# Kernel optimization log

Hardware: AMD Instinct MI355X
Metric: run time of the kernel (lower is better)

## Reference

```python
import jax, jax.numpy as jnp
import numpy as np

B, T = 16384, 512          # batch, seq_len
DSTATE, DINPUT = 4, 4       # quaternion state / quaternion input
DMLP1, DMLP2 = 128, 128     # ODEFunc MLP hidden widths


def _linear_params(key, fan_in, fan_out):
    # torch nn.Linear default init: U(-1/sqrt(fan_in), 1/sqrt(fan_in))
    lim = 1.0 / np.sqrt(fan_in)
    kw, kb = jax.random.split(key)
    W = jax.random.uniform(kw, (fan_in, fan_out), jnp.float32, -lim, lim)
    b = jax.random.uniform(kb, (fan_out,), jnp.float32, -lim, lim)
    return W, b


def setup_inputs() -> dict:
    key = jax.random.key(0)
    k1, k2, k3, kx = jax.random.split(key, 4)
    W1, b1 = _linear_params(k1, DSTATE + DINPUT, DMLP1)
    W2, b2 = _linear_params(k2, DMLP1, DMLP2)
    W3, b3 = _linear_params(k3, DMLP2, DSTATE)
    quat_seq = jax.random.normal(kx, (B, T, DINPUT), jnp.float32)
    return {"quat_seq": quat_seq, "W1": W1, "b1": b1, "W2": W2, "b2": b2,
            "W3": W3, "b3": b3}


def reference(quat_seq, W1, b1, W2, b2, W3, b3):
    batch = quat_seq.shape[0]
    dstate = W3.shape[1]

    def odefunc(h, q):
        # f(t, [h, q]) -> dh/dt ; time is unused by the net
        x = jnp.concatenate([h, q], axis=-1)            # [B, DSTATE+DINPUT]
        x = jax.nn.silu(x @ W1 + b1)                    # [B, DMLP1]
        x = jax.nn.silu(x @ W2 + b2)                    # [B, DMLP2]
        return x @ W3 + b3                              # [B, DSTATE]

    dt = 1.0  # t_span = [0, 1] on a fixed grid -> single RK4 step of size 1

    def step(h, q_t):
        # torchdiffeq fixed-grid 'rk4' uses the 3/8-rule (rk4_alt_step_func)
        k1 = odefunc(h, q_t)
        k2 = odefunc(h + dt * k1 / 3.0, q_t)
        k3 = odefunc(h + dt * (k2 - k1 / 3.0), q_t)
        k4 = odefunc(h + dt * (k1 - k2 + k3), q_t)
        h_new = h + dt * (k1 + 3.0 * (k2 + k3) + k4) / 8.0
        return h_new, None

    h0 = jnp.zeros((batch, dstate), quat_seq.dtype).at[:, 0].set(1.0)
    # scan over time: [T, B, DINPUT]
    h_final, _ = jax.lax.scan(step, h0, jnp.swapaxes(quat_seq, 0, 1))
    return h_final
```

## Files before the change

### kernel.cpp

```cpp
#include <hip/hip_runtime.h>
#include <hip/hip_bf16.h>

typedef float f32x4  __attribute__((ext_vector_type(4)));
typedef float f32x16 __attribute__((ext_vector_type(16)));
typedef short short8v __attribute__((ext_vector_type(8)));
typedef unsigned int uint;

constexpr int TSTEPS = 512;

union FragU { uint u[4]; short8v v; };

__device__ __forceinline__ float silu_f(float x) {
    return __fdividef(x, 1.0f + __expf(-x));
}

__device__ __forceinline__ uint bf16_rne(float x) {
    uint ux = __float_as_uint(x);
    return (ux + 0x7FFFu + ((ux >> 16) & 1u)) & 0xFFFF0000u;
}
__device__ __forceinline__ void split2u(float x, uint &h, uint &l) {
    h = bf16_rne(x);
    float rem = x - __uint_as_float(h);
    l = bf16_rne(rem);
}

__device__ __forceinline__ uint cvtpk(float a, float b) {
    union { __hip_bfloat162 h; uint u; } cv;
    cv.h = __float22bfloat162_rn(make_float2(a, b));
    return cv.u;
}
__device__ __forceinline__ void split4_pk(const f32x4 v, uint2 &hi, uint2 &lo) {
    hi.x = cvtpk(v.x, v.y);
    hi.y = cvtpk(v.z, v.w);
    float h0 = __uint_as_float(hi.x << 16);
    float h1 = __uint_as_float(hi.x & 0xFFFF0000u);
    float h2 = __uint_as_float(hi.y << 16);
    float h3 = __uint_as_float(hi.y & 0xFFFF0000u);
    lo.x = cvtpk(v.x - h0, v.y - h1);
    lo.y = cvtpk(v.z - h2, v.w - h3);
}

#define SX1(lev,kt,gk,b) (((((lev)*8+(kt))*2+(gk))*32+(b))*8)

__global__ __launch_bounds__(256, 2)
void odernn_v8(const float* __restrict__ quat,
               const float* __restrict__ W1, const float* __restrict__ b1,
               const float* __restrict__ W2, const float* __restrict__ b2,
               const float* __restrict__ W3, const float* __restrict__ b3,
               float* __restrict__ out)
{
    __shared__ short sx1[2 * 8 * 2 * 32 * 8];
    __shared__ float sb1[128];
    __shared__ float sb2[128];
    __shared__ float sW3[512];
    __shared__ float sk3[4][32][4];

    const int tid  = threadIdx.x;
    const int w    = tid >> 6;
    const int lane = tid & 63;
    const int b    = lane & 31;
    const int gp   = lane >> 5;
    const int rowbase = blockIdx.x * 32;

    if (tid < 128) { sb1[tid] = b1[tid]; sb2[tid] = b2[tid]; }
    for (int i = tid; i < 512; i += 256) sW3[i] = W3[i];

    short8v A2[8][2];
#pragma unroll
    for (int kt = 0; kt < 8; ++kt) {
#pragma unroll
        for (int e = 0; e < 8; ++e) {
            float x = W2[(16 * kt + 8 * gp + e) * 128 + (32 * w + b)];
            uint h, l; split2u(x, h, l);
            A2[kt][0][e] = (short)(h >> 16);
            A2[kt][1][e] = (short)(l >> 16);
        }
    }
    short8v A1;
#pragma unroll
    for (int e = 0; e < 8; ++e) {
        float x = W1[e * 128 + (32 * w + b)];
        uint h, l; split2u(x, h, l);
        A1[e] = (short)((gp ? l : h) >> 16);
    }
    f32x4 b3v = *(const f32x4*)b3;

    __syncthreads();

    f32x4 h  = {1.0f, 0, 0, 0};
    f32x4 k1 = {0,0,0,0}, k2 = {0,0,0,0}, k3v = {0,0,0,0};
    const float* qp = quat + (size_t)(rowbase + b) * TSTEPS * 4;

#pragma unroll 1
    for (int t = 0; t < TSTEPS; ++t) {
        f32x4 q = *(const f32x4*)(qp + 4 * t);
        uint2 qhi, qlo;
        split4_pk(q, qhi, qlo);
        f32x4 hnew = {0,0,0,0};

#pragma unroll
        for (int s = 0; s < 4; ++s) {
            f32x4 hs = h;
            if (s == 1)      hs += k1 * (1.0f/3.0f);
            else if (s == 2) hs += k2 - k1 * (1.0f/3.0f);
            else if (s == 3) hs += k1 - k2 + k3v;

            uint2 hhi, hlo;
            split4_pk(hs, hhi, hlo);
            FragU b0a, b0b;
            b0a.u[0] = gp ? hlo.x : hhi.x;  b0a.u[1] = gp ? hlo.y : hhi.y;
            b0a.u[2] = gp ? qlo.x : qhi.x;  b0a.u[3] = gp ? qlo.y : qhi.y;
            b0b.u[0] = gp ? hhi.x : hlo.x;  b0b.u[1] = gp ? hhi.y : hlo.y;
            b0b.u[2] = gp ? qhi.x : qlo.x;  b0b.u[3] = gp ? qhi.y : qlo.y;

            f32x16 c1;
#pragma unroll
            for (int qd = 0; qd < 4; ++qd) {
                f32x4 bv = *(const f32x4*)&sb1[32 * w + 8 * qd + 4 * gp];
                c1[4*qd+0] = bv.x; c1[4*qd+1] = bv.y;
                c1[4*qd+2] = bv.z; c1[4*qd+3] = bv.w;
            }
            c1 = __builtin_amdgcn_mfma_f32_32x32x16_bf16(A1, b0a.v, c1, 0, 0, 0);
            c1 = __builtin_amdgcn_mfma_f32_32x32x16_bf16(A1, b0b.v, c1, 0, 0, 0);

#pragma unroll
            for (int qd = 0; qd < 4; ++qd) {
                f32x4 sv;
                sv.x = silu_f(c1[4*qd+0]); sv.y = silu_f(c1[4*qd+1]);
                sv.z = silu_f(c1[4*qd+2]); sv.w = silu_f(c1[4*qd+3]);
                uint2 phi, plo;
                split4_pk(sv, phi, plo);
                const int kt = 2 * w + (qd >> 1);
                const int gk = qd & 1;
                *(uint2*)&sx1[SX1(0, kt, gk, b) + 4 * gp] = phi;
                *(uint2*)&sx1[SX1(1, kt, gk, b) + 4 * gp] = plo;
            }
            __syncthreads();

            f32x16 c2;
#pragma unroll
            for (int qd = 0; qd < 4; ++qd) {
                f32x4 bv = *(const f32x4*)&sb2[32 * w + 8 * qd + 4 * gp];
                c2[4*qd+0] = bv.x; c2[4*qd+1] = bv.y;
                c2[4*qd+2] = bv.z; c2[4*qd+3] = bv.w;
            }
#pragma unroll
            for (int kt = 0; kt < 8; ++kt) {
                short8v Bh = *(const short8v*)&sx1[SX1(0, kt, gp, b)];
                short8v Bl = *(const short8v*)&sx1[SX1(1, kt, gp, b)];
                c2 = __builtin_amdgcn_mfma_f32_32x32x16_bf16(A2[kt][1], Bl, c2, 0, 0, 0);
                c2 = __builtin_amdgcn_mfma_f32_32x32x16_bf16(A2[kt][1], Bh, c2, 0, 0, 0);
                c2 = __builtin_amdgcn_mfma_f32_32x32x16_bf16(A2[kt][0], Bl, c2, 0, 0, 0);
                c2 = __builtin_amdgcn_mfma_f32_32x32x16_bf16(A2[kt][0], Bh, c2, 0, 0, 0);
            }

            f32x4 p = {0,0,0,0};
#pragma unroll
            for (int i = 0; i < 16; ++i) {
                const int j = 32 * w + 8 * (i >> 2) + (i & 3) + 4 * gp;
                const float xv = silu_f(c2[i]);
                p += xv * (*(const f32x4*)&sW3[j * 4]);
            }
            p.x += __shfl_xor(p.x, 32, 64);
            p.y += __shfl_xor(p.y, 32, 64);
            p.z += __shfl_xor(p.z, 32, 64);
            p.w += __shfl_xor(p.w, 32, 64);
            if (lane < 32) *(f32x4*)&sk3[w][lane][0] = p;
            __syncthreads();

            f32x4 ks = b3v;
#pragma unroll
            for (int w2 = 0; w2 < 4; ++w2)
                ks += *(const f32x4*)&sk3[w2][b][0];

            const float wgt = (s == 1 || s == 2) ? 0.375f : 0.125f;
            hnew += ks * wgt;
            if (s == 0)      k1  = ks;
            else if (s == 1) k2  = ks;
            else if (s == 2) k3v = ks;
        }
        h += hnew;
    }

    if (tid < 32)
        *(f32x4*)&out[(size_t)(rowbase + tid) * 4] = h;
}

extern "C" void kernel_launch(void* const* d_in, const int* in_sizes, int n_in,
                              void* d_out, int out_size, void* d_ws, size_t ws_size,
                              hipStream_t stream)
{
    const float* quat = (const float*)d_in[0];
    const float* W1   = (const float*)d_in[1];
    const float* b1   = (const float*)d_in[2];
    const float* W2   = (const float*)d_in[3];
    const float* b2   = (const float*)d_in[4];
    const float* W3   = (const float*)d_in[5];
    const float* b3   = (const float*)d_in[6];
    float* out        = (float*)d_out;

    const int B = in_sizes[0] / (TSTEPS * 4);
    dim3 grid(B / 32), block(256);
    hipLaunchKernelGGL(odernn_v8, grid, block, 0, stream,
                       quat, W1, b1, W2, b2, W3, b3, out);
}
```

Measured before the change: 7.385 ms.

## Ping-pong two 32-row groups per block so layer-1 and layer-2 phases overlap

Each block of 512 threads now holds two independent 32-row groups (roles) that run the per-stage work as two phases (layer 1, then layer 2 plus the output projection), offset by one half-step. On every barrier one role does layer 1 while the other does layer 2, so their MFMA and SiLU work can interleave. The goal is to hide the latency of the serial MFMA chains and barriers. The layer-2 accumulation is also split into two independent accumulators so the dependent MFMA chain is shorter. The cost is a barrier that now spans 8 waves, one block per CU through the new launch bounds, and extra register pressure.

```diff
diff --git a/kernel.cpp b/kernel.cpp
--- a/kernel.cpp
+++ b/kernel.cpp
@@ -7,6 +7,7 @@
 typedef unsigned int uint;
 
 constexpr int TSTEPS = 512;
+constexpr int NSTAGE = TSTEPS * 4;
 
 union FragU { uint u[4]; short8v v; };
 
@@ -42,28 +43,30 @@
 
 #define SX1(lev,kt,gk,b) (((((lev)*8+(kt))*2+(gk))*32+(b))*8)
 
-__global__ __launch_bounds__(256, 2)
-void odernn_v8(const float* __restrict__ quat,
+__global__ __launch_bounds__(512, 1)
+void odernn_v9(const float* __restrict__ quat,
                const float* __restrict__ W1, const float* __restrict__ b1,
                const float* __restrict__ W2, const float* __restrict__ b2,
                const float* __restrict__ W3, const float* __restrict__ b3,
                float* __restrict__ out)
 {
-    __shared__ short sx1[2 * 8 * 2 * 32 * 8];
+    __shared__ short sx1[2][2 * 8 * 2 * 32 * 8];
     __shared__ float sb1[128];
     __shared__ float sb2[128];
     __shared__ float sW3[512];
-    __shared__ float sk3[4][32][4];
+    __shared__ float sk3[2][4][32][4];
 
     const int tid  = threadIdx.x;
-    const int w    = tid >> 6;
+    const int wave = tid >> 6;
+    const int role = wave >> 2;
+    const int w    = wave & 3;
     const int lane = tid & 63;
     const int b    = lane & 31;
     const int gp   = lane >> 5;
-    const int rowbase = blockIdx.x * 32;
+    const int rowbase = blockIdx.x * 64 + role * 32;
 
     if (tid < 128) { sb1[tid] = b1[tid]; sb2[tid] = b2[tid]; }
-    for (int i = tid; i < 512; i += 256) sW3[i] = W3[i];
+    if (tid < 512) sW3[tid] = W3[tid];
 
     short8v A2[8][2];
 #pragma unroll
@@ -71,119 +74,139 @@
 #pragma unroll
         for (int e = 0; e < 8; ++e) {
             float x = W2[(16 * kt + 8 * gp + e) * 128 + (32 * w + b)];
-            uint h, l; split2u(x, h, l);
-            A2[kt][0][e] = (short)(h >> 16);
-            A2[kt][1][e] = (short)(l >> 16);
+            uint h2_, l2_; split2u(x, h2_, l2_);
+            A2[kt][0][e] = (short)(h2_ >> 16);
+            A2[kt][1][e] = (short)(l2_ >> 16);
         }
     }
     short8v A1;
 #pragma unroll
     for (int e = 0; e < 8; ++e) {
         float x = W1[e * 128 + (32 * w + b)];
-        uint h, l; split2u(x, h, l);
-        A1[e] = (short)((gp ? l : h) >> 16);
+        uint h1_, l1_; split2u(x, h1_, l1_);
+        A1[e] = (short)((gp ? l1_ : h1_) >> 16);
     }
     f32x4 b3v = *(const f32x4*)b3;
 
     __syncthreads();
 
-    f32x4 h  = {1.0f, 0, 0, 0};
-    f32x4 k1 = {0,0,0,0}, k2 = {0,0,0,0}, k3v = {0,0,0,0};
+    const f32x4 Z4 = {0.0f, 0.0f, 0.0f, 0.0f};
+    f32x4 h  = {1.0f, 0.0f, 0.0f, 0.0f};
+    f32x4 hnew = Z4, k1 = Z4, k2 = Z4, k3v = Z4, q = Z4;
+    uint2 qhi = {0, 0}, qlo = {0, 0};
     const float* qp = quat + (size_t)(rowbase + b) * TSTEPS * 4;
-
-#pragma unroll 1
-    for (int t = 0; t < TSTEPS; ++t) {
-        f32x4 q = *(const f32x4*)(qp + 4 * t);
-        uint2 qhi, qlo;
-        split4_pk(q, qhi, qlo);
-        f32x4 hnew = {0,0,0,0};
-
-#pragma unroll
-        for (int s = 0; s < 4; ++s) {
-            f32x4 hs = h;
-            if (s == 1)      hs += k1 * (1.0f/3.0f);
-            else if (s == 2) hs += k2 - k1 * (1.0f/3.0f);
-            else if (s == 3) hs += k1 - k2 + k3v;
-
-            uint2 hhi, hlo;
-            split4_pk(hs, hhi, hlo);
-            FragU b0a, b0b;
-            b0a.u[0] = gp ? hlo.x : hhi.x;  b0a.u[1] = gp ? hlo.y : hhi.y;
-            b0a.u[2] = gp ? qlo.x : qhi.x;  b0a.u[3] = gp ? qlo.y : qhi.y;
-            b0b.u[0] = gp ? hhi.x : hlo.x;  b0b.u[1] = gp ? hhi.y : hlo.y;
-            b0b.u[2] = gp ? qhi.x : qlo.x;  b0b.u[3] = gp ? qhi.y : qlo.y;
-
-            f32x16 c1;
-#pragma unroll
-            for (int qd = 0; qd < 4; ++qd) {
-                f32x4 bv = *(const f32x4*)&sb1[32 * w + 8 * qd + 4 * gp];
-                c1[4*qd+0] = bv.x; c1[4*qd+1] = bv.y;
-                c1[4*qd+2] = bv.z; c1[4*qd+3] = bv.w;
+    short* const sx1g = &sx1[role][0];
+
+    auto P1 = [&](int s) {
+        if (s > 0) {
+            const int sp = (s - 1) & 3;
+            f32x4 ks = b3v;
+#pragma unroll
+            for (int w2 = 0; w2 < 4; ++w2)
+                ks += *(const f32x4*)&sk3[role][w2][b][0];
+            const float wgt = (sp == 1 || sp == 2) ? 0.375f : 0.125f;
+            hnew += ks * wgt;
+            if (sp == 0)      k1  = ks;
+            else if (sp == 1) k2  = ks;
+            else if (sp == 2) k3v = ks;
+            else { h += hnew; hnew = Z4; }
+        }
+        if (s >= NSTAGE) return;
+        const int sub = s & 3;
+        if (sub == 0) {
+            q = *(const f32x4*)(qp + (size_t)(s >> 2) * 4);
+            split4_pk(q, qhi, qlo);
+        }
+        f32x4 hs = h;
+        if (sub == 1)      hs += k1 * (1.0f / 3.0f);
+        else if (sub == 2) hs += k2 - k1 * (1.0f / 3.0f);
+        else if (sub == 3) hs += k1 - k2 + k3v;
+
+        uint2 hhi, hlo;
+        split4_pk(hs, hhi, hlo);
+        FragU b0a, b0b;
+        b0a.u[0] = gp ? hlo.x : hhi.x;  b0a.u[1] = gp ? hlo.y : hhi.y;
+        b0a.u[2] = gp ? qlo.x : qhi.x;  b0a.u[3] = gp ? qlo.y : qhi.y;
+        b0b.u[0] = gp ? hhi.x : hlo.x;  b0b.u[1] = gp ? hhi.y : hlo.y;
+        b0b.u[2] = gp ? qhi.x : qlo.x;  b0b.u[3] = gp ? qhi.y : qlo.y;
+
+        f32x16 c1;
+#pragma unroll
+        for (int qd = 0; qd < 4; ++qd) {
+            f32x4 bv = *(const f32x4*)&sb1[32 * w + 8 * qd + 4 * gp];
+            c1[4*qd+0] = bv.x; c1[4*qd+1] = bv.y;
+            c1[4*qd+2] = bv.z; c1[4*qd+3] = bv.w;
+        }
+        c1 = __builtin_amdgcn_mfma_f32_32x32x16_bf16(A1, b0a.v, c1, 0, 0, 0);
+        c1 = __builtin_amdgcn_mfma_f32_32x32x16_bf16(A1, b0b.v, c1, 0, 0, 0);
+
+#pragma unroll
+        for (int qd = 0; qd < 4; ++qd) {
+            f32x4 sv;
+            sv.x = silu_f(c1[4*qd+0]); sv.y = silu_f(c1[4*qd+1]);
+            sv.z = silu_f(c1[4*qd+2]); sv.w = silu_f(c1[4*qd+3]);
+            uint2 phi, plo;
+            split4_pk(sv, phi, plo);
+            const int kt = 2 * w + (qd >> 1);
+            const int gk = qd & 1;
+            *(uint2*)&sx1g[SX1(0, kt, gk, b) + 4 * gp] = phi;
+            *(uint2*)&sx1g[SX1(1, kt, gk, b) + 4 * gp] = plo;
+        }
+    };
+
+    auto P2 = [&](int s) {
+        (void)s;
+        f32x16 u, vv;
+#pragma unroll
+        for (int qd = 0; qd < 4; ++qd) {
+            f32x4 bv = *(const f32x4*)&sb2[32 * w + 8 * qd + 4 * gp];
+            u[4*qd+0] = bv.x; u[4*qd+1] = bv.y;
+            u[4*qd+2] = bv.z; u[4*qd+3] = bv.w;
+        }
+#pragma unroll
+        for (int i = 0; i < 16; ++i) vv[i] = 0.0f;
+#pragma unroll
+        for (int kt = 0; kt < 8; ++kt) {
+            short8v Bh = *(const short8v*)&sx1g[SX1(0, kt, gp, b)];
+            short8v Bl = *(const short8v*)&sx1g[SX1(1, kt, gp, b)];
+            if (kt & 1) {
+                vv = __builtin_amdgcn_mfma_f32_32x32x16_bf16(A2[kt][1], Bl, vv, 0, 0, 0);
+                vv = __builtin_amdgcn_mfma_f32_32x32x16_bf16(A2[kt][1], Bh, vv, 0, 0, 0);
+                vv = __builtin_amdgcn_mfma_f32_32x32x16_bf16(A2[kt][0], Bl, vv, 0, 0, 0);
+                vv = __builtin_amdgcn_mfma_f32_32x32x16_bf16(A2[kt][0], Bh, vv, 0, 0, 0);
+            } else {
+                u = __builtin_amdgcn_mfma_f32_32x32x16_bf16(A2[kt][1], Bl, u, 0, 0, 0);
+                u = __builtin_amdgcn_mfma_f32_32x32x16_bf16(A2[kt][1], Bh, u, 0, 0, 0);
+                u = __builtin_amdgcn_mfma_f32_32x32x16_bf16(A2[kt][0], Bl, u, 0, 0, 0);
+                u = __builtin_amdgcn_mfma_f32_32x32x16_bf16(A2[kt][0], Bh, u, 0, 0, 0);
             }
-            c1 = __builtin_amdgcn_mfma_f32_32x32x16_bf16(A1, b0a.v, c1, 0, 0, 0);
-            c1 = __builtin_amdgcn_mfma_f32_32x32x16_bf16(A1, b0b.v, c1, 0, 0, 0);
-
-#pragma unroll
-            for (int qd = 0; qd < 4; ++qd) {
-                f32x4 sv;
-                sv.x = silu_f(c1[4*qd+0]); sv.y = silu_f(c1[4*qd+1]);
-                sv.z = silu_f(c1[4*qd+2]); sv.w = silu_f(c1[4*qd+3]);
-                uint2 phi, plo;
-                split4_pk(sv, phi, plo);
-                const int kt = 2 * w + (qd >> 1);
-                const int gk = qd & 1;
-                *(uint2*)&sx1[SX1(0, kt, gk, b) + 4 * gp] = phi;
-                *(uint2*)&sx1[SX1(1, kt, gk, b) + 4 * gp] = plo;
-            }
-            __syncthreads();
-
-            f32x16 c2;
-#pragma unroll
-            for (int qd = 0; qd < 4; ++qd) {
-                f32x4 bv = *(const f32x4*)&sb2[32 * w + 8 * qd + 4 * gp];
-                c2[4*qd+0] = bv.x; c2[4*qd+1] = bv.y;
-                c2[4*qd+2] = bv.z; c2[4*qd+3] = bv.w;
-            }
-#pragma unroll
-            for (int kt = 0; kt < 8; ++kt) {
-                short8v Bh = *(const short8v*)&sx1[SX1(0, kt, gp, b)];
-                short8v Bl = *(const short8v*)&sx1[SX1(1, kt, gp, b)];
-                c2 = __builtin_amdgcn_mfma_f32_32x32x16_bf16(A2[kt][1], Bl, c2, 0, 0, 0);
-                c2 = __builtin_amdgcn_mfma_f32_32x32x16_bf16(A2[kt][1], Bh, c2, 0, 0, 0);
-                c2 = __builtin_amdgcn_mfma_f32_32x32x16_bf16(A2[kt][0], Bl, c2, 0, 0, 0);
-                c2 = __builtin_amdgcn_mfma_f32_32x32x16_bf16(A2[kt][0], Bh, c2, 0, 0, 0);
-            }
-
-            f32x4 p = {0,0,0,0};
-#pragma unroll
-            for (int i = 0; i < 16; ++i) {
-                const int j = 32 * w + 8 * (i >> 2) + (i & 3) + 4 * gp;
-                const float xv = silu_f(c2[i]);
-                p += xv * (*(const f32x4*)&sW3[j * 4]);
-            }
-            p.x += __shfl_xor(p.x, 32, 64);
-            p.y += __shfl_xor(p.y, 32, 64);
-            p.z += __shfl_xor(p.z, 32, 64);
-            p.w += __shfl_xor(p.w, 32, 64);
-            if (lane < 32) *(f32x4*)&sk3[w][lane][0] = p;
-            __syncthreads();
-
-            f32x4 ks = b3v;
-#pragma unroll
-            for (int w2 = 0; w2 < 4; ++w2)
-                ks += *(const f32x4*)&sk3[w2][b][0];
-
-            const float wgt = (s == 1 || s == 2) ? 0.375f : 0.125f;
-            hnew += ks * wgt;
-            if (s == 0)      k1  = ks;
-            else if (s == 1) k2  = ks;
-            else if (s == 2) k3v = ks;
-        }
-        h += hnew;
+        }
+
+        f32x4 p = {0.0f, 0.0f, 0.0f, 0.0f};
+#pragma unroll
+        for (int i = 0; i < 16; ++i) {
+            const int j = 32 * w + 8 * (i >> 2) + (i & 3) + 4 * gp;
+            const float xv = silu_f(u[i] + vv[i]);
+            p += xv * (*(const f32x4*)&sW3[j * 4]);
+        }
+        p.x += __shfl_xor(p.x, 32, 64);
+        p.y += __shfl_xor(p.y, 32, 64);
+        p.z += __shfl_xor(p.z, 32, 64);
+        p.w += __shfl_xor(p.w, 32, 64);
+        if (lane < 32) *(f32x4*)&sk3[role][w][lane][0] = p;
+    };
+
+    for (int hi = 0; hi < 2 * NSTAGE + 2; ++hi) {
+        const int myhi = hi - role;
+        if (myhi >= 0 && myhi <= 2 * NSTAGE) {
+            if ((myhi & 1) == 0) P1(myhi >> 1);
+            else                 P2(myhi >> 1);
+        }
+        __syncthreads();
     }
 
-    if (tid < 32)
-        *(f32x4*)&out[(size_t)(rowbase + tid) * 4] = h;
+    if (w == 0 && lane < 32)
+        *(f32x4*)&out[(size_t)(rowbase + lane) * 4] = h;
 }
 
 extern "C" void kernel_launch(void* const* d_in, const int* in_sizes, int n_in,
@@ -200,7 +223,7 @@
     float* out        = (float*)d_out;
 
     const int B = in_sizes[0] / (TSTEPS * 4);
-    dim3 grid(B / 32), block(256);
-    hipLaunchKernelGGL(odernn_v8, grid, block, 0, stream,
+    dim3 grid(B / 64), block(512);
+    hipLaunchKernelGGL(odernn_v9, grid, block, 0, stream,
                        quat, W1, b1, W2, b2, W3, b3, out);
 }
```

New measurement: 8.208 ms. 1.11x slower.

## Drop lo*lo MFMA term, split layer-2 accumulation chains, keep W3 in registers

Applied to the files above, without the earlier changes.

Layer 2 previously used four MFMAs per k-tile, one per pairing of the hi and lo bf16 halves. It now skips the lo*lo product, leaving three MFMAs per k-tile. Those are spread across two independent accumulators (even and odd k-tiles) that are summed before the SiLU, which breaks the serial dependency chain through the MFMA pipeline. W3 moves from shared memory into 16 registers per thread, and the next step's quaternion input is prefetched one iteration ahead. Dropping lo*lo slightly lowers precision, and the extra registers (A2 is already large) raise spill and occupancy risk under launch_bounds(256,2).

```diff
diff --git a/kernel.cpp b/kernel.cpp
--- a/kernel.cpp
+++ b/kernel.cpp
@@ -43,16 +43,15 @@
 #define SX1(lev,kt,gk,b) (((((lev)*8+(kt))*2+(gk))*32+(b))*8)
 
 __global__ __launch_bounds__(256, 2)
-void odernn_v8(const float* __restrict__ quat,
-               const float* __restrict__ W1, const float* __restrict__ b1,
-               const float* __restrict__ W2, const float* __restrict__ b2,
-               const float* __restrict__ W3, const float* __restrict__ b3,
-               float* __restrict__ out)
+void odernn_v10(const float* __restrict__ quat,
+                const float* __restrict__ W1, const float* __restrict__ b1,
+                const float* __restrict__ W2, const float* __restrict__ b2,
+                const float* __restrict__ W3, const float* __restrict__ b3,
+                float* __restrict__ out)
 {
     __shared__ short sx1[2 * 8 * 2 * 32 * 8];
     __shared__ float sb1[128];
     __shared__ float sb2[128];
-    __shared__ float sW3[512];
     __shared__ float sk3[4][32][4];
 
     const int tid  = threadIdx.x;
@@ -63,7 +62,6 @@
     const int rowbase = blockIdx.x * 32;
 
     if (tid < 128) { sb1[tid] = b1[tid]; sb2[tid] = b2[tid]; }
-    for (int i = tid; i < 512; i += 256) sW3[i] = W3[i];
 
     short8v A2[8][2];
 #pragma unroll
@@ -71,17 +69,23 @@
 #pragma unroll
         for (int e = 0; e < 8; ++e) {
             float x = W2[(16 * kt + 8 * gp + e) * 128 + (32 * w + b)];
-            uint h, l; split2u(x, h, l);
-            A2[kt][0][e] = (short)(h >> 16);
-            A2[kt][1][e] = (short)(l >> 16);
+            uint h2_, l2_; split2u(x, h2_, l2_);
+            A2[kt][0][e] = (short)(h2_ >> 16);
+            A2[kt][1][e] = (short)(l2_ >> 16);
         }
     }
     short8v A1;
 #pragma unroll
     for (int e = 0; e < 8; ++e) {
         float x = W1[e * 128 + (32 * w + b)];
-        uint h, l; split2u(x, h, l);
-        A1[e] = (short)((gp ? l : h) >> 16);
+        uint h1_, l1_; split2u(x, h1_, l1_);
+        A1[e] = (short)((gp ? l1_ : h1_) >> 16);
+    }
+    f32x4 W3r[16];
+#pragma unroll
+    for (int i = 0; i < 16; ++i) {
+        const int j = 32 * w + 8 * (i >> 2) + (i & 3) + 4 * gp;
+        W3r[i] = *(const f32x4*)&W3[j * 4];
     }
     f32x4 b3v = *(const f32x4*)b3;
 
@@ -91,9 +95,14 @@
     f32x4 k1 = {0,0,0,0}, k2 = {0,0,0,0}, k3v = {0,0,0,0};
     const float* qp = quat + (size_t)(rowbase + b) * TSTEPS * 4;
 
+    f32x4 qnext = *(const f32x4*)qp;
+
 #pragma unroll 1
     for (int t = 0; t < TSTEPS; ++t) {
-        f32x4 q = *(const f32x4*)(qp + 4 * t);
+        const f32x4 q = qnext;
+        const int tn = (t + 1 < TSTEPS) ? t + 1 : t;
+        qnext = *(const f32x4*)(qp + 4 * tn);
+
         uint2 qhi, qlo;
         split4_pk(q, qhi, qlo);
         f32x4 hnew = {0,0,0,0};
@@ -137,29 +146,35 @@
             }
             __syncthreads();
 
-            f32x16 c2;
+            f32x16 u, vv;
 #pragma unroll
             for (int qd = 0; qd < 4; ++qd) {
                 f32x4 bv = *(const f32x4*)&sb2[32 * w + 8 * qd + 4 * gp];
-                c2[4*qd+0] = bv.x; c2[4*qd+1] = bv.y;
-                c2[4*qd+2] = bv.z; c2[4*qd+3] = bv.w;
-            }
+                u[4*qd+0] = bv.x; u[4*qd+1] = bv.y;
+                u[4*qd+2] = bv.z; u[4*qd+3] = bv.w;
+            }
+#pragma unroll
+            for (int i = 0; i < 16; ++i) vv[i] = 0.0f;
 #pragma unroll
             for (int kt = 0; kt < 8; ++kt) {
                 short8v Bh = *(const short8v*)&sx1[SX1(0, kt, gp, b)];
                 short8v Bl = *(const short8v*)&sx1[SX1(1, kt, gp, b)];
-                c2 = __builtin_amdgcn_mfma_f32_32x32x16_bf16(A2[kt][1], Bl, c2, 0, 0, 0);
-                c2 = __builtin_amdgcn_mfma_f32_32x32x16_bf16(A2[kt][1], Bh, c2, 0, 0, 0);
-                c2 = __builtin_amdgcn_mfma_f32_32x32x16_bf16(A2[kt][0], Bl, c2, 0, 0, 0);
-                c2 = __builtin_amdgcn_mfma_f32_32x32x16_bf16(A2[kt][0], Bh, c2, 0, 0, 0);
-            }
-
-            f32x4 p = {0,0,0,0};
+                if (kt & 1) {
+                    vv = __builtin_amdgcn_mfma_f32_32x32x16_bf16(A2[kt][1], Bh, vv, 0, 0, 0);
+                    vv = __builtin_amdgcn_mfma_f32_32x32x16_bf16(A2[kt][0], Bl, vv, 0, 0, 0);
+                    vv = __builtin_amdgcn_mfma_f32_32x32x16_bf16(A2[kt][0], Bh, vv, 0, 0, 0);
+                } else {
+                    u = __builtin_amdgcn_mfma_f32_32x32x16_bf16(A2[kt][1], Bh, u, 0, 0, 0);
+                    u = __builtin_amdgcn_mfma_f32_32x32x16_bf16(A2[kt][0], Bl, u, 0, 0, 0);
+                    u = __builtin_amdgcn_mfma_f32_32x32x16_bf16(A2[kt][0], Bh, u, 0, 0, 0);
+                }
+            }
+
+            f32x4 p = {0.0f, 0.0f, 0.0f, 0.0f};
 #pragma unroll
             for (int i = 0; i < 16; ++i) {
-                const int j = 32 * w + 8 * (i >> 2) + (i & 3) + 4 * gp;
-                const float xv = silu_f(c2[i]);
-                p += xv * (*(const f32x4*)&sW3[j * 4]);
+                const float xv = silu_f(u[i] + vv[i]);
+                p += xv * W3r[i];
             }
             p.x += __shfl_xor(p.x, 32, 64);
             p.y += __shfl_xor(p.y, 32, 64);
@@ -201,6 +216,6 @@
 
     const int B = in_sizes[0] / (TSTEPS * 4);
     dim3 grid(B / 32), block(256);
-    hipLaunchKernelGGL(odernn_v8, grid, block, 0, stream,
+    hipLaunchKernelGGL(odernn_v10, grid, block, 0, stream,
                        quat, W1, b1, W2, b2, W3, b3, out);
 }
```

After: 6.753 ms. 8.6% less time.
